# Kernel tuning notes

Measured on AMD Instinct MI355X. Metric: run time of the kernel, lower is better.

## Reference

```python
import jax, jax.numpy as jnp
import numpy as np

N, C, H, W = 4, 256, 64, 64
E = C // 2  # embed_dim = max(C//2, 1)


def setup_inputs() -> dict:
    key = jax.random.key(0)
    k1, k2, k3, k4 = jax.random.split(key, 4)
    x = jax.random.normal(k1, (N, C, H, W), dtype=jnp.float32)
    # 1x1 conv weights == channel-mixing matrices (bias=False), std=0.01 init
    W_theta = jax.random.normal(k2, (E, C), dtype=jnp.float32) * 0.01
    W_phi = jax.random.normal(k3, (E, C), dtype=jnp.float32) * 0.01
    W_proj = jax.random.normal(k4, (C, C), dtype=jnp.float32) * 0.01  # zero_init=False
    return {"x": x, "W_theta": W_theta, "W_phi": W_phi, "W_proj": W_proj}


def reference(x, W_theta, W_phi, W_proj):
    n, c, h, w = x.shape
    s = h * w
    xf = x.reshape(n, c, s)                      # [N, C, S]
    theta = jnp.einsum('ec,ncs->nes', W_theta, xf)  # [N, E, S]
    phi = jnp.einsum('ec,ncs->nes', W_phi, xf)      # [N, E, S]
    # f = theta^T @ phi, scaled by sqrt(embed_dim) (theta.shape[-1] after permute)
    scale = jnp.sqrt(jnp.asarray(theta.shape[1], dtype=x.dtype))
    f = jnp.einsum('nes,net->nst', theta, phi) / scale  # [N, S, S]
    f = jax.nn.softmax(f, axis=-1)
    # y = f @ g^T with g = x (unembedded values)
    y = jnp.einsum('nst,nct->ncs', f, xf)        # [N, C, S]
    residual = jnp.einsum('oc,ncs->nos', W_proj, y).reshape(n, c, h, w)
    return x + residual
```

## Files before the change

### kernel.cpp

```cpp
#include <hip/hip_runtime.h>
#include <cmath>

#define C_DIM 256
#define E_DIM 128
#define S_DIM 4096

typedef __bf16 bf16x8 __attribute__((ext_vector_type(8)));
typedef float  f32x4  __attribute__((ext_vector_type(4)));
typedef short  s16x8  __attribute__((ext_vector_type(8)));
typedef short  s16x4  __attribute__((ext_vector_type(4)));

__device__ __forceinline__ unsigned short f2bf(float f) {
  union { float f; unsigned u; } v; v.f = f;
  unsigned r = v.u + 0x7FFFu + ((v.u >> 16) & 1u);
  return (unsigned short)(r >> 16);
}
__device__ __forceinline__ unsigned short f2bf_tr(float f) {
  union { float f; unsigned u; } v; v.f = f;
  return (unsigned short)(v.u >> 16);
}
__device__ __forceinline__ bf16x8 as_bf(s16x8 v) {
  union { s16x8 s; bf16x8 b; } u; u.s = v; return u.b;
}
__device__ __forceinline__ bf16x8 f2b8(f32x4 v) { union { f32x4 f; bf16x8 b; } u; u.f = v; return u.b; }
__device__ __forceinline__ f32x4 b2f8(bf16x8 v) { union { bf16x8 b; f32x4 f; } u; u.b = v; return u.f; }
__device__ __forceinline__ f32x4 s2f8(s16x8 v)  { union { s16x8 s; f32x4 f; } u; u.s = v; return u.f; }
__device__ __forceinline__ s16x8 f2s8(f32x4 v)  { union { f32x4 f; s16x8 s; } u; u.f = v; return u.s; }

#define MFMA16(a, b, c) __builtin_amdgcn_mfma_f32_16x16x32_bf16(a, b, c, 0, 0, 0)

__global__ __launch_bounds__(256) void cast_w_kernel(
    const float* __restrict__ Wth, const float* __restrict__ Wph,
    const float* __restrict__ Wpr, short* __restrict__ Wb) {
  int t = blockIdx.x * 256 + threadIdx.x;
  int i = t * 4;
  const float* src; int j;
  if (i < 32768)      { src = Wth; j = i; }
  else if (i < 65536) { src = Wph; j = i - 32768; }
  else                { src = Wpr; j = i - 65536; }
  float4 v = *(const float4*)(src + j);
  s16x4 o;
  o[0] = (short)f2bf(v.x); o[1] = (short)f2bf(v.y);
  o[2] = (short)f2bf(v.z); o[3] = (short)f2bf(v.w);
  *(s16x4*)(Wb + i) = o;
}

__global__ __launch_bounds__(256) void mix_kernel(
    const float* __restrict__ x, const short* __restrict__ Wb,
    short* __restrict__ Qg, short* __restrict__ Kg, short* __restrict__ Xb,
    float qscale) {
  __shared__ short lxT[32 * C_DIM];
  int bid = blockIdx.x;
  int n = bid >> 7, s0 = (bid & 127) * 32;
  int tid = threadIdx.x;
  int wid = tid >> 6, lane = tid & 63, l15 = lane & 15, l4 = lane >> 4;

  {
    int cp = tid >> 1, su = tid & 1;
    const float* r0 = x + ((size_t)n * C_DIM + 2 * cp) * S_DIM + s0 + su * 16;
    const float* r1 = r0 + S_DIM;
    float a0[16], a1[16];
    #pragma unroll
    for (int j = 0; j < 4; ++j) {
      *(float4*)(a0 + 4 * j) = *(const float4*)(r0 + 4 * j);
      *(float4*)(a1 + 4 * j) = *(const float4*)(r1 + 4 * j);
    }
    short b0[16], b1[16];
    #pragma unroll
    for (int j = 0; j < 16; ++j) { b0[j] = (short)f2bf(a0[j]); b1[j] = (short)f2bf(a1[j]); }
    short* xb0 = Xb + ((size_t)n * C_DIM + 2 * cp) * S_DIM + s0 + su * 16;
    *(s16x8*)(xb0)             = *(s16x8*)(b0);
    *(s16x8*)(xb0 + 8)         = *(s16x8*)(b0 + 8);
    *(s16x8*)(xb0 + S_DIM)     = *(s16x8*)(b1);
    *(s16x8*)(xb0 + S_DIM + 8) = *(s16x8*)(b1 + 8);
    #pragma unroll
    for (int j = 0; j < 16; ++j) {
      int s = su * 16 + j;
      unsigned d = (unsigned)(unsigned short)b0[j] |
                   ((unsigned)(unsigned short)b1[j] << 16);
      *(unsigned*)((char*)lxT + s * 512 + ((4 * cp) ^ ((s & 7) << 4))) = d;
    }
  }
  __syncthreads();

  const short* Wq = Wb;
  const short* Wk = Wb + 32768;
  const f32x4 fzero = {0.f, 0.f, 0.f, 0.f};
  f32x4 accQ[2][2], accK[2][2];
  #pragma unroll
  for (int a = 0; a < 2; ++a)
    #pragma unroll
    for (int b = 0; b < 2; ++b) { accQ[a][b] = fzero; accK[a][b] = fzero; }

  #pragma unroll 2
  for (int kk = 0; kk < 8; ++kk) {
    bf16x8 bfr[2];
    #pragma unroll
    for (int nf = 0; nf < 2; ++nf) {
      int s = nf * 16 + l15;
      bfr[nf] = *(const bf16x8*)((char*)lxT + s * 512 +
                                 ((kk * 64 + l4 * 16) ^ ((s & 7) << 4)));
    }
    #pragma unroll
    for (int mf = 0; mf < 2; ++mf) {
      int e = wid * 32 + mf * 16 + l15;
      bf16x8 aq = *(const bf16x8*)(Wq + e * C_DIM + kk * 32 + l4 * 8);
      bf16x8 ak = *(const bf16x8*)(Wk + e * C_DIM + kk * 32 + l4 * 8);
      #pragma unroll
      for (int nf = 0; nf < 2; ++nf) {
        accQ[mf][nf] = MFMA16(aq, bfr[nf], accQ[mf][nf]);
        accK[mf][nf] = MFMA16(ak, bfr[nf], accK[mf][nf]);
      }
    }
  }

  #pragma unroll
  for (int mf = 0; mf < 2; ++mf) {
    #pragma unroll
    for (int nf = 0; nf < 2; ++nf) {
      int e = wid * 32 + mf * 16 + l4 * 4;
      int s = s0 + nf * 16 + l15;
      s16x4 pq, pk;
      #pragma unroll
      for (int r = 0; r < 4; ++r) {
        pq[r] = (short)f2bf(accQ[mf][nf][r] * qscale);
        pk[r] = (short)f2bf(accK[mf][nf][r]);
      }
      *(s16x4*)(Qg + ((size_t)n * S_DIM + s) * E_DIM + e) = pq;
      *(s16x4*)(Kg + ((size_t)n * S_DIM + s) * E_DIM + e) = pk;
    }
  }
}


#define QF(qs, ec) f2b8(RA[(qs) * 4 + (ec)])

#define QKT_BODY(B)                                                           \
  {                                                                           \
    const char* kb = (const char*)lK + (B) * 16384;                           \
    char* pw = (char*)lP + (B) * 8192;                                        \
    RB[0] = fzero; RB[1] = fzero; RB[2] = fzero; RB[3] = fzero;               \
    int trow = tq * 16 + l15;                                                 \
    int swz = (trow & 7) << 4;                                                \
    __builtin_amdgcn_s_setprio(1);                                            \
    _Pragma("unroll")                                                         \
    for (int ec = 0; ec < 4; ++ec) {                                          \
      bf16x8 kf = *(const bf16x8*)(kb + trow * 256 + ((ec * 64 + l4 * 16) ^ swz)); \
      _Pragma("unroll")                                                       \
      for (int qs = 0; qs < 4; ++qs)                                          \
        RB[qs] = MFMA16(kf, QF(qs, ec), RB[qs]);                              \
    }                                                                         \
    __builtin_amdgcn_s_setprio(0);                                            \
    int tb2 = tq * 32 + l4 * 8;                                               \
    _Pragma("unroll")                                                         \
    for (int qs = 0; qs < 4; ++qs) {                                          \
      float p0 = __builtin_amdgcn_exp2f(RB[qs][0]);                           \
      float p1 = __builtin_amdgcn_exp2f(RB[qs][1]);                           \
      float p2 = __builtin_amdgcn_exp2f(RB[qs][2]);                           \
      float p3 = __builtin_amdgcn_exp2f(RB[qs][3]);                           \
      lsum[qs] += (p0 + p1) + (p2 + p3);                                      \
      uint2 dd;                                                               \
      dd.x = (unsigned)f2bf_tr(p0) | ((unsigned)f2bf_tr(p1) << 16);           \
      dd.y = (unsigned)f2bf_tr(p2) | ((unsigned)f2bf_tr(p3) << 16);           \
      int q = qs * 16 + l15;                                                  \
      *(uint2*)(pw + q * 128 + (tb2 ^ ((q & 7) << 4))) = dd;                  \
    }                                                                         \
  }

#define PV_VISSUE(OFF, TI)                                                    \
  _Pragma("unroll")                                                           \
  for (int kk = 0; kk < 2; ++kk)                                              \
    _Pragma("unroll")                                                         \
    for (int ct = 0; ct < 4; ++ct)                                            \
      RA[(OFF) + kk * 4 + ct] = s2f8(*(const s16x8*)(                         \
          Vb + (size_t)(cq * 64 + ct * 16 + l15) * S_DIM + (TI) * 64 + kk * 32 + l4 * 8));

#define PV_KCOMMIT(OFF, B)                                                    \
  {                                                                           \
    char* kw = (char*)lK + (B) * 16384;                                       \
    _Pragma("unroll")                                                         \
    for (int jj = 0; jj < 4; ++jj) {                                          \
      int r = kr + 16 * jj;                                                   \
      *(s16x8*)(kw + r * 256 + ((kc * 16) ^ ((r & 7) << 4))) = f2s8(RB[(OFF) + jj]); \
    }                                                                         \
  }

#define PV_KLOAD(OFF, TI)                                                     \
  _Pragma("unroll")                                                           \
  for (int jj = 0; jj < 4; ++jj)                                              \
    RB[(OFF) + jj] = s2f8(*(const s16x8*)(                                    \
        Kb + (size_t)((TI) * 64 + kr + 16 * jj) * E_DIM + kc * 8));

#define PV_MFMA(OFF, PBUF)                                                    \
  {                                                                           \
    const char* pr = (const char*)lP + (PBUF) * 8192;                         \
    _Pragma("unroll")                                                         \
    for (int kk = 0; kk < 2; ++kk) {                                          \
      bf16x8 pf[4];                                                           \
      _Pragma("unroll")                                                       \
      for (int qs = 0; qs < 4; ++qs) {                                        \
        int q = qs * 16 + l15;                                                \
        pf[qs] = *(const bf16x8*)(pr + q * 128 + ((kk * 64 + l4 * 16) ^ ((q & 7) << 4))); \
      }                                                                       \
      __builtin_amdgcn_s_setprio(1);                                          \
      _Pragma("unroll")                                                       \
      for (int ct = 0; ct < 4; ++ct) {                                        \
        bf16x8 vf = as_bf(f2s8(RA[(OFF) + kk * 4 + ct]));                     \
        _Pragma("unroll")                                                     \
        for (int qs = 0; qs < 4; ++qs)                                        \
          acc[qs][ct] = MFMA16(pf[qs], vf, acc[qs][ct]);                      \
      }                                                                       \
      __builtin_amdgcn_s_setprio(0);                                          \
    }                                                                         \
  }

#define RAW_BARRIER()                                                         \
  asm volatile("s_waitcnt lgkmcnt(0)" ::: "memory");                          \
  __builtin_amdgcn_s_barrier();

__global__ __launch_bounds__(512, 2) void attn_kernel(
    const short* __restrict__ Qg, const short* __restrict__ Kg,
    const short* __restrict__ Xb, const short* __restrict__ Wpb,
    const float* __restrict__ xg, float* __restrict__ out) {
  __shared__ short lK[2 * 64 * E_DIM];
  __shared__ short lP[2 * 64 * 64];
  __shared__ float lsred[4 * 64];

  int bid = blockIdx.x;
  int xcd = bid & 7;
  int n   = xcd >> 1;
  int s0  = (((xcd & 1) << 5) + (bid >> 3)) * 64;

  int tid = threadIdx.x;
  int wid = tid >> 6, lane = tid & 63;
  int l15 = lane & 15, l4 = lane >> 4;

  const short* Kb = Kg + (size_t)n * S_DIM * E_DIM;
  const short* Vb = Xb + (size_t)n * (size_t)C_DIM * S_DIM;

  const f32x4 fzero = {0.f, 0.f, 0.f, 0.f};

  f32x4 RA[16];
  f32x4 RB[8];
  float lsum[4];
  f32x4 acc[4][4];

  int tq = wid;
  int cq = wid - 4;
  int idx = tid & 255;
  int kr = idx >> 4, kc = idx & 15;

  if (wid < 4) {
    #pragma unroll
    for (int qs = 0; qs < 4; ++qs) {
      const short* qp = Qg + ((size_t)n * S_DIM + s0 + qs * 16 + l15) * E_DIM + l4 * 8;
      #pragma unroll
      for (int ec = 0; ec < 4; ++ec) RA[qs * 4 + ec] = b2f8(*(const bf16x8*)(qp + ec * 32));
    }
    #pragma unroll
    for (int j = 0; j < 4; ++j) lsum[j] = 0.f;
  } else {
    #pragma unroll
    for (int a = 0; a < 4; ++a)
      #pragma unroll
      for (int b = 0; b < 4; ++b) acc[a][b] = fzero;
    PV_KLOAD(0, 0);
    PV_KCOMMIT(0, 0);
    PV_KLOAD(4, 1);
    PV_VISSUE(0, 0);
  }
  RAW_BARRIER();

  for (int j = 0; j < 32; ++j) {
    int i0 = 2 * j;
    if (wid < 4) {
      QKT_BODY(0);
    } else {
      if (j > 0)  PV_VISSUE(0, i0);
      PV_KCOMMIT(4, 1);
      if (j > 0)  PV_MFMA(8, 1);
      if (j < 31) PV_KLOAD(0, i0 + 2);
    }
    RAW_BARRIER();
    if (wid < 4) {
      QKT_BODY(1);
    } else {
      PV_VISSUE(8, i0 + 1);
      if (j < 31) PV_KCOMMIT(0, 0);
      PV_MFMA(0, 0);
      if (j < 31) PV_KLOAD(4, i0 + 3);
    }
    RAW_BARRIER();
  }
  if (wid >= 4) {
    PV_MFMA(8, 1);
  }

  if (wid < 4) {
    #pragma unroll
    for (int qs = 0; qs < 4; ++qs) {
      float v = lsum[qs];
      v += __shfl_xor(v, 16);
      v += __shfl_xor(v, 32);
      if (lane < 16) lsred[tq * 64 + qs * 16 + l15] = v;
    }
  }
  __syncthreads();

  char* yst = (char*)lK;
  if (wid >= 4) {
    #pragma unroll
    for (int qs = 0; qs < 4; ++qs) {
      #pragma unroll
      for (int r = 0; r < 4; ++r) {
        int q = qs * 16 + l4 * 4 + r;
        float tot = lsred[q] + lsred[64 + q] + lsred[128 + q] + lsred[192 + q];
        float rl = 1.0f / tot;
        #pragma unroll
        for (int ct = 0; ct < 4; ++ct) {
          int c = cq * 64 + ct * 16 + l15;
          *(unsigned short*)(yst + q * 512 + ((c * 2) ^ ((q & 7) << 4))) =
              f2bf_tr(acc[qs][ct][r] * rl);
        }
      }
    }
  }
  __syncthreads();

  {
    f32x4 pacc[4][2];
    #pragma unroll
    for (int a = 0; a < 4; ++a)
      #pragma unroll
      for (int b = 0; b < 2; ++b) pacc[a][b] = fzero;

    #pragma unroll 2
    for (int kk = 0; kk < 8; ++kk) {
      bf16x8 af[4];
      #pragma unroll
      for (int mf = 0; mf < 4; ++mf) {
        int q = mf * 16 + l15;
        af[mf] = *(const bf16x8*)(yst + q * 512 + ((kk * 64 + l4 * 16) ^ ((q & 7) << 4)));
      }
      #pragma unroll
      for (int nf = 0; nf < 2; ++nf) {
        int o = wid * 32 + nf * 16 + l15;
        bf16x8 bfr = *(const bf16x8*)(Wpb + o * C_DIM + kk * 32 + l4 * 8);
        #pragma unroll
        for (int mf = 0; mf < 4; ++mf)
          pacc[mf][nf] = MFMA16(af[mf], bfr, pacc[mf][nf]);
      }
    }

    #pragma unroll
    for (int mf = 0; mf < 4; ++mf) {
      #pragma unroll
      for (int nf = 0; nf < 2; ++nf) {
        int o = wid * 32 + nf * 16 + l15;
        size_t idx2 = ((size_t)n * C_DIM + o) * (size_t)S_DIM + s0 + mf * 16 + l4 * 4;
        float4 xv = *(const float4*)(xg + idx2);
        float4 r;
        r.x = xv.x + pacc[mf][nf][0];
        r.y = xv.y + pacc[mf][nf][1];
        r.z = xv.z + pacc[mf][nf][2];
        r.w = xv.w + pacc[mf][nf][3];
        *(float4*)(out + idx2) = r;
      }
    }
  }
}

extern "C" void kernel_launch(void* const* d_in, const int* in_sizes, int n_in,
                              void* d_out, int out_size, void* d_ws, size_t ws_size,
                              hipStream_t stream) {
  const float* x   = (const float*)d_in[0];
  const float* Wth = (const float*)d_in[1];
  const float* Wph = (const float*)d_in[2];
  const float* Wpr = (const float*)d_in[3];
  float* out = (float*)d_out;

  short* q_ws  = (short*)d_ws;
  short* k_ws  = q_ws  + (size_t)4 * S_DIM * E_DIM;
  short* xb_ws = k_ws  + (size_t)4 * S_DIM * E_DIM;
  short* wb_ws = xb_ws + (size_t)4 * C_DIM * S_DIM;

  float qscale = 1.4426950408889634f / sqrtf(128.0f);

  cast_w_kernel<<<128, 256, 0, stream>>>(Wth, Wph, Wpr, wb_ws);
  mix_kernel<<<512, 256, 0, stream>>>(x, wb_ws, q_ws, k_ws, xb_ws, qscale);
  attn_kernel<<<256, 512, 0, stream>>>(q_ws, k_ws, xb_ws, wb_ws + 65536, x, out);
}
```

Measured before the change: 108.2 us.

## Use FP8 for P and V in the PV matmul of attention

Stores the unembedded values X and the softmax probabilities P as FP8 (e4m3 via cvt_pk_fp8) instead of bf16, and runs the P·V product with the 16x16x32 fp8 MFMA. This halves the V global reads, the P LDS traffic and the register staging for V. The aim is to relieve memory and LDS bandwidth in the attention inner loop. It risks accuracy loss: FP8 has few mantissa bits and unnormalised exp2 values can exceed e4m3 range, though the small projection weights damp the error in the residual.

```diff
diff --git a/kernel.cpp b/kernel.cpp
--- a/kernel.cpp
+++ b/kernel.cpp
@@ -9,6 +9,7 @@
 typedef float  f32x4  __attribute__((ext_vector_type(4)));
 typedef short  s16x8  __attribute__((ext_vector_type(8)));
 typedef short  s16x4  __attribute__((ext_vector_type(4)));
+typedef long long llx2 __attribute__((ext_vector_type(2)));
 
 __device__ __forceinline__ unsigned short f2bf(float f) {
   union { float f; unsigned u; } v; v.f = f;
@@ -26,6 +27,13 @@
 __device__ __forceinline__ f32x4 b2f8(bf16x8 v) { union { bf16x8 b; f32x4 f; } u; u.b = v; return u.f; }
 __device__ __forceinline__ f32x4 s2f8(s16x8 v)  { union { s16x8 s; f32x4 f; } u; u.s = v; return u.f; }
 __device__ __forceinline__ s16x8 f2s8(f32x4 v)  { union { f32x4 f; s16x8 s; } u; u.f = v; return u.s; }
+__device__ __forceinline__ llx2 f2ll(f32x4 v)   { union { f32x4 f; llx2 l; } u; u.f = v; return u.l; }
+__device__ __forceinline__ f32x4 ll2f(llx2 v)   { union { llx2 l; f32x4 f; } u; u.l = v; return u.f; }
+__device__ __forceinline__ unsigned pk8(float x0, float x1, float x2, float x3) {
+  int d = __builtin_amdgcn_cvt_pk_fp8_f32(x0, x1, 0, false);
+  d = __builtin_amdgcn_cvt_pk_fp8_f32(x2, x3, d, true);
+  return (unsigned)d;
+}
 
 #define MFMA16(a, b, c) __builtin_amdgcn_mfma_f32_16x16x32_bf16(a, b, c, 0, 0, 0)
 
@@ -47,8 +55,8 @@
 
 __global__ __launch_bounds__(256) void mix_kernel(
     const float* __restrict__ x, const short* __restrict__ Wb,
-    short* __restrict__ Qg, short* __restrict__ Kg, short* __restrict__ Xb,
-    float qscale) {
+    short* __restrict__ Qg, short* __restrict__ Kg,
+    unsigned char* __restrict__ Xb8, float qscale) {
   __shared__ short lxT[32 * C_DIM];
   int bid = blockIdx.x;
   int n = bid >> 7, s0 = (bid & 127) * 32;
@@ -65,19 +73,22 @@
       *(float4*)(a0 + 4 * j) = *(const float4*)(r0 + 4 * j);
       *(float4*)(a1 + 4 * j) = *(const float4*)(r1 + 4 * j);
     }
-    short b0[16], b1[16];
-    #pragma unroll
-    for (int j = 0; j < 16; ++j) { b0[j] = (short)f2bf(a0[j]); b1[j] = (short)f2bf(a1[j]); }
-    short* xb0 = Xb + ((size_t)n * C_DIM + 2 * cp) * S_DIM + s0 + su * 16;
-    *(s16x8*)(xb0)             = *(s16x8*)(b0);
-    *(s16x8*)(xb0 + 8)         = *(s16x8*)(b0 + 8);
-    *(s16x8*)(xb0 + S_DIM)     = *(s16x8*)(b1);
-    *(s16x8*)(xb0 + S_DIM + 8) = *(s16x8*)(b1 + 8);
+    unsigned char* xb0 = Xb8 + ((size_t)n * C_DIM + 2 * cp) * S_DIM + s0 + su * 16;
+    uint4 w0, w1;
+    w0.x = pk8(a0[0], a0[1], a0[2], a0[3]);
+    w0.y = pk8(a0[4], a0[5], a0[6], a0[7]);
+    w0.z = pk8(a0[8], a0[9], a0[10], a0[11]);
+    w0.w = pk8(a0[12], a0[13], a0[14], a0[15]);
+    w1.x = pk8(a1[0], a1[1], a1[2], a1[3]);
+    w1.y = pk8(a1[4], a1[5], a1[6], a1[7]);
+    w1.z = pk8(a1[8], a1[9], a1[10], a1[11]);
+    w1.w = pk8(a1[12], a1[13], a1[14], a1[15]);
+    *(uint4*)(xb0) = w0;
+    *(uint4*)(xb0 + S_DIM) = w1;
     #pragma unroll
     for (int j = 0; j < 16; ++j) {
       int s = su * 16 + j;
-      unsigned d = (unsigned)(unsigned short)b0[j] |
-                   ((unsigned)(unsigned short)b1[j] << 16);
+      unsigned d = (unsigned)f2bf(a0[j]) | ((unsigned)f2bf(a1[j]) << 16);
       *(unsigned*)((char*)lxT + s * 512 + ((4 * cp) ^ ((s & 7) << 4))) = d;
     }
   }
@@ -138,7 +149,7 @@
 #define QKT_BODY(B)                                                           \
   {                                                                           \
     const char* kb = (const char*)lK + (B) * 16384;                           \
-    char* pw = (char*)lP + (B) * 8192;                                        \
+    char* pw = (char*)lP + (B) * 4096;                                        \
     RB[0] = fzero; RB[1] = fzero; RB[2] = fzero; RB[3] = fzero;               \
     int trow = tq * 16 + l15;                                                 \
     int swz = (trow & 7) << 4;                                                \
@@ -151,7 +162,7 @@
         RB[qs] = MFMA16(kf, QF(qs, ec), RB[qs]);                              \
     }                                                                         \
     __builtin_amdgcn_s_setprio(0);                                            \
-    int tb2 = tq * 32 + l4 * 8;                                               \
+    int tb1 = tq * 16 + l4 * 4;                                               \
     _Pragma("unroll")                                                         \
     for (int qs = 0; qs < 4; ++qs) {                                          \
       float p0 = __builtin_amdgcn_exp2f(RB[qs][0]);                           \
@@ -159,21 +170,21 @@
       float p2 = __builtin_amdgcn_exp2f(RB[qs][2]);                           \
       float p3 = __builtin_amdgcn_exp2f(RB[qs][3]);                           \
       lsum[qs] += (p0 + p1) + (p2 + p3);                                      \
-      uint2 dd;                                                               \
-      dd.x = (unsigned)f2bf_tr(p0) | ((unsigned)f2bf_tr(p1) << 16);           \
-      dd.y = (unsigned)f2bf_tr(p2) | ((unsigned)f2bf_tr(p3) << 16);           \
       int q = qs * 16 + l15;                                                  \
-      *(uint2*)(pw + q * 128 + (tb2 ^ ((q & 7) << 4))) = dd;                  \
+      *(unsigned*)(pw + q * 64 + (tb1 ^ ((q & 7) << 3))) = pk8(p0, p1, p2, p3); \
     }                                                                         \
   }
 
 #define PV_VISSUE(OFF, TI)                                                    \
   _Pragma("unroll")                                                           \
-  for (int kk = 0; kk < 2; ++kk)                                              \
-    _Pragma("unroll")                                                         \
-    for (int ct = 0; ct < 4; ++ct)                                            \
-      RA[(OFF) + kk * 4 + ct] = s2f8(*(const s16x8*)(                         \
-          Vb + (size_t)(cq * 64 + ct * 16 + l15) * S_DIM + (TI) * 64 + kk * 32 + l4 * 8));
+  for (int j = 0; j < 8; ++j) {                                               \
+    long long t_ = *(const long long*)(                                       \
+        Vb + (size_t)(cq * 64 + (j & 3) * 16 + l15) * S_DIM +                 \
+        (TI) * 64 + (j >> 2) * 32 + l4 * 8);                                  \
+    llx2 r_ = f2ll(RA[(OFF) + (j >> 1)]);                                     \
+    r_[j & 1] = t_;                                                           \
+    RA[(OFF) + (j >> 1)] = ll2f(r_);                                          \
+  }
 
 #define PV_KCOMMIT(OFF, B)                                                    \
   {                                                                           \
@@ -193,22 +204,23 @@
 
 #define PV_MFMA(OFF, PBUF)                                                    \
   {                                                                           \
-    const char* pr = (const char*)lP + (PBUF) * 8192;                         \
+    const char* pr = (const char*)lP + (PBUF) * 4096;                         \
     _Pragma("unroll")                                                         \
     for (int kk = 0; kk < 2; ++kk) {                                          \
-      bf16x8 pf[4];                                                           \
+      long long pf[4];                                                        \
       _Pragma("unroll")                                                       \
       for (int qs = 0; qs < 4; ++qs) {                                        \
         int q = qs * 16 + l15;                                                \
-        pf[qs] = *(const bf16x8*)(pr + q * 128 + ((kk * 64 + l4 * 16) ^ ((q & 7) << 4))); \
+        pf[qs] = *(const long long*)(pr + q * 64 + ((kk * 32 + l4 * 8) ^ ((q & 7) << 3))); \
       }                                                                       \
       __builtin_amdgcn_s_setprio(1);                                          \
       _Pragma("unroll")                                                       \
       for (int ct = 0; ct < 4; ++ct) {                                        \
-        bf16x8 vf = as_bf(f2s8(RA[(OFF) + kk * 4 + ct]));                     \
+        long long vf = f2ll(RA[(OFF) + ((kk * 4 + ct) >> 1)])[(kk * 4 + ct) & 1]; \
         _Pragma("unroll")                                                     \
         for (int qs = 0; qs < 4; ++qs)                                        \
-          acc[qs][ct] = MFMA16(pf[qs], vf, acc[qs][ct]);                      \
+          acc[qs][ct] = __builtin_amdgcn_mfma_f32_16x16x32_fp8_fp8(           \
+              pf[qs], vf, acc[qs][ct], 0, 0, 0);                              \
       }                                                                       \
       __builtin_amdgcn_s_setprio(0);                                          \
     }                                                                         \
@@ -220,10 +232,10 @@
 
 __global__ __launch_bounds__(512, 2) void attn_kernel(
     const short* __restrict__ Qg, const short* __restrict__ Kg,
-    const short* __restrict__ Xb, const short* __restrict__ Wpb,
+    const unsigned char* __restrict__ Xb8, const short* __restrict__ Wpb,
     const float* __restrict__ xg, float* __restrict__ out) {
   __shared__ short lK[2 * 64 * E_DIM];
-  __shared__ short lP[2 * 64 * 64];
+  __shared__ char  lP[2 * 64 * 64];
   __shared__ float lsred[4 * 64];
 
   int bid = blockIdx.x;
@@ -236,7 +248,7 @@
   int l15 = lane & 15, l4 = lane >> 4;
 
   const short* Kb = Kg + (size_t)n * S_DIM * E_DIM;
-  const short* Vb = Xb + (size_t)n * (size_t)C_DIM * S_DIM;
+  const unsigned char* Vb = Xb8 + (size_t)n * (size_t)C_DIM * S_DIM;
 
   const f32x4 fzero = {0.f, 0.f, 0.f, 0.f};
 
@@ -278,14 +290,14 @@
     } else {
       if (j > 0)  PV_VISSUE(0, i0);
       PV_KCOMMIT(4, 1);
-      if (j > 0)  PV_MFMA(8, 1);
+      if (j > 0)  PV_MFMA(4, 1);
       if (j < 31) PV_KLOAD(0, i0 + 2);
     }
     RAW_BARRIER();
     if (wid < 4) {
       QKT_BODY(1);
     } else {
-      PV_VISSUE(8, i0 + 1);
+      PV_VISSUE(4, i0 + 1);
       if (j < 31) PV_KCOMMIT(0, 0);
       PV_MFMA(0, 0);
       if (j < 31) PV_KLOAD(4, i0 + 3);
@@ -293,7 +305,7 @@
     RAW_BARRIER();
   }
   if (wid >= 4) {
-    PV_MFMA(8, 1);
+    PV_MFMA(4, 1);
   }
 
   if (wid < 4) {
@@ -380,13 +392,13 @@
   float* out = (float*)d_out;
 
   short* q_ws  = (short*)d_ws;
-  short* k_ws  = q_ws  + (size_t)4 * S_DIM * E_DIM;
-  short* xb_ws = k_ws  + (size_t)4 * S_DIM * E_DIM;
-  short* wb_ws = xb_ws + (size_t)4 * C_DIM * S_DIM;
+  short* k_ws  = q_ws + (size_t)4 * S_DIM * E_DIM;
+  unsigned char* xb8_ws = (unsigned char*)(k_ws + (size_t)4 * S_DIM * E_DIM);
+  short* wb_ws = (short*)(xb8_ws + (size_t)4 * C_DIM * S_DIM);
 
   float qscale = 1.4426950408889634f / sqrtf(128.0f);
 
   cast_w_kernel<<<128, 256, 0, stream>>>(Wth, Wph, Wpr, wb_ws);
-  mix_kernel<<<512, 256, 0, stream>>>(x, wb_ws, q_ws, k_ws, xb_ws, qscale);
-  attn_kernel<<<256, 512, 0, stream>>>(q_ws, k_ws, xb_ws, wb_ws + 65536, x, out);
-}
+  mix_kernel<<<512, 256, 0, stream>>>(x, wb_ws, q_ws, k_ws, xb8_ws, qscale);
+  attn_kernel<<<256, 512, 0, stream>>>(q_ws, k_ws, xb8_ws, wb_ws + 65536, x, out);
+}
```

Result: faster. 104.9 us, median of 2 (-3.1%).
